# Optimization experiments

Hardware: AMD Instinct MI355X
Metric: run time of the kernel (lower is better)

## Reference

```python
import jax, jax.numpy as jnp
import numpy as np

N_NODES = 50000
N_EDGES = 600000
D = 128
THETA = (0.5, -1.0, 0.5)  # len(theta) must be 3 to match learnable_diag[3, in_feats]


def setup_inputs() -> dict:
    key = jax.random.key(0)
    k1, k2, k3, k4, k5 = jax.random.split(key, 5)
    feat = jax.random.normal(k1, (N_NODES, D), dtype=jnp.float32)
    edge_index = jax.random.randint(k2, (2, N_EDGES), 0, N_NODES)  # [src; dst]
    # learnable_diag = torch.rand(3, in_feats)
    diag = jax.random.uniform(k3, (3, D), dtype=jnp.float32)
    # nn.Linear(out_feats, out_feats) with xavier_uniform weight, zero bias
    limit = float(np.sqrt(6.0 / (D + D)))
    W = jax.random.uniform(k4, (D, D), dtype=jnp.float32, minval=-limit, maxval=limit)
    b = jnp.zeros((D,), dtype=jnp.float32)
    return {"feat": feat, "edge_index": edge_index, "diag": diag, "W": W, "b": b}


def reference(feat, edge_index, diag, W, b):
    src, dst = edge_index[0], edge_index[1]
    n = feat.shape[0]
    # in_degrees: count of incoming edges per node
    deg = jax.ops.segment_sum(jnp.ones_like(dst, dtype=feat.dtype), dst, num_segments=n)
    d_invsqrt = jnp.clip(deg, 1.0, None) ** -0.5  # [N]
    d_invsqrt = d_invsqrt[:, None]  # [N,1]

    h = (THETA[0] * feat) * diag[0]
    h = h @ W.T + b  # nn.Linear

    for k in range(1, len(THETA)):
        # unnLaplacian: feat - (A @ (feat * Dinv)) * Dinv * diag[k]
        msg = feat * d_invsqrt  # [N,D]
        agg = jax.ops.segment_sum(msg[src], dst, num_segments=n)  # SpMM: copy_u + sum
        feat = feat - agg * d_invsqrt * diag[k]
        h = h + THETA[k] * feat
    return h
```

## Files before the change

### kernel.cpp

```cpp
#include <hip/hip_runtime.h>

#define NN 50000
#define NE 600000
#define D  128
#define NBLK 196

typedef __attribute__((ext_vector_type(8))) short bf16x8;
typedef __attribute__((ext_vector_type(4))) float floatx4;

__device__ __forceinline__ unsigned short bf16_rne(float f) {
    union { float f; unsigned u; } v; v.f = f;
    unsigned r = v.u + 0x7FFFu + ((v.u >> 16) & 1u);
    return (unsigned short)(r >> 16);
}

__global__ __launch_bounds__(256) void hist_kernel(const int* __restrict__ dst,
                                                   int* __restrict__ deg_i) {
    int e = blockIdx.x * 256 + threadIdx.x;
    if (e < NE) atomicAdd(&deg_i[dst[e]], 1);
}

__global__ __launch_bounds__(256) void scan1_kernel(const int* __restrict__ deg_i,
                                                    int* __restrict__ row_ptr,
                                                    int* __restrict__ partials,
                                                    float* __restrict__ dinvf) {
    __shared__ int sh[256];
    int i = blockIdx.x * 256 + threadIdx.x;
    int dg = (i < NN) ? deg_i[i] : 0;
    if (i < NN) {
        float d = (float)dg;
        dinvf[i] = rsqrtf(d > 1.0f ? d : 1.0f);
    }
    sh[threadIdx.x] = dg;
    __syncthreads();
    #pragma unroll
    for (int off = 1; off < 256; off <<= 1) {
        int t = (threadIdx.x >= off) ? sh[threadIdx.x - off] : 0;
        __syncthreads();
        sh[threadIdx.x] += t;
        __syncthreads();
    }
    if (i < NN) row_ptr[i + 1] = sh[threadIdx.x];
    if (threadIdx.x == 255) partials[blockIdx.x] = sh[255];
}

__global__ __launch_bounds__(256) void scan2_kernel(int* __restrict__ partials) {
    __shared__ int sh[256];
    sh[threadIdx.x] = (threadIdx.x < NBLK) ? partials[threadIdx.x] : 0;
    __syncthreads();
    #pragma unroll
    for (int off = 1; off < 256; off <<= 1) {
        int t = (threadIdx.x >= off) ? sh[threadIdx.x - off] : 0;
        __syncthreads();
        sh[threadIdx.x] += t;
        __syncthreads();
    }
    if (threadIdx.x < NBLK) partials[threadIdx.x] = sh[threadIdx.x];
}

__global__ __launch_bounds__(256) void scan3_kernel(int* __restrict__ row_ptr,
                                                    const int* __restrict__ partials,
                                                    int* __restrict__ fillc) {
    int i = blockIdx.x * 256 + threadIdx.x;
    if (i < NN) {
        int add = (blockIdx.x > 0) ? partials[blockIdx.x - 1] : 0;
        row_ptr[i + 1] += add;
        fillc[i] = 0;
    }
    if (i == 0) row_ptr[0] = 0;
}

__global__ __launch_bounds__(256) void fill_kernel(const int* __restrict__ src,
                                                   const int* __restrict__ dst,
                                                   const int* __restrict__ row_ptr,
                                                   const float* __restrict__ dinvf,
                                                   int* __restrict__ fillc,
                                                   int2* __restrict__ csr) {
    int e = blockIdx.x * 256 + threadIdx.x;
    if (e < NE) {
        int t = dst[e];
        int s = src[e];
        int pos = row_ptr[t] + atomicAdd(&fillc[t], 1);
        csr[pos] = make_int2(s, __float_as_int(dinvf[s]));
    }
}

__global__ __launch_bounds__(256) void cvt_kernel(const float* __restrict__ feat,
                                                  unsigned int* __restrict__ featb) {
    int idx = blockIdx.x * 256 + threadIdx.x;
    const float4 f = ((const float4*)feat)[idx];
    unsigned int lo = (unsigned)bf16_rne(f.x) | ((unsigned)bf16_rne(f.y) << 16);
    unsigned int hi = (unsigned)bf16_rne(f.z) | ((unsigned)bf16_rne(f.w) << 16);
    ((uint2*)featb)[idx] = make_uint2(lo, hi);
}

__device__ __forceinline__ float2 gather_acc(const unsigned short* __restrict__ featb,
                                             const int2* __restrict__ csr,
                                             int e0, int e1, int lane) {
    float2 acc = make_float2(0.0f, 0.0f);
    for (int bse = e0; bse < e1; bse += 64) {
        int idx = bse + lane;
        int s = 0;
        float w = 0.0f;
        if (idx < e1) {
            int2 p = csr[idx];
            s = p.x;
            w = __int_as_float(p.y);
        }
        int cnt4 = (min(64, e1 - bse) + 3) & ~3;
        for (int k = 0; k < cnt4; k += 4) {
            #pragma unroll
            for (int u = 0; u < 4; ++u) {
                int   ss = __shfl(s, k + u);
                float ww = __shfl(w, k + u);
                unsigned pv = *(const unsigned*)(featb + (size_t)ss * D + 2 * lane);
                acc.x += __uint_as_float(pv << 16) * ww;
                acc.y += __uint_as_float(pv & 0xFFFF0000u) * ww;
            }
        }
    }
    return acc;
}

__global__ __launch_bounds__(256) void gather1_kernel(const unsigned short* __restrict__ featb,
                                                      const int2* __restrict__ csr,
                                                      const int* __restrict__ row_ptr,
                                                      const float* __restrict__ dinvf,
                                                      const float* __restrict__ diag,
                                                      const float* __restrict__ feat0,
                                                      unsigned int* __restrict__ feat1b) {
    const int node = blockIdx.x * 4 + (threadIdx.x >> 6);
    const int lane = threadIdx.x & 63;
    float2 acc = gather_acc(featb, csr, row_ptr[node], row_ptr[node + 1], lane);

    const size_t o2 = (size_t)node * (D / 2) + lane;
    const float di = dinvf[node];
    const float2 bs = *(const float2*)&feat0[2 * o2];
    const float2 dg = *(const float2*)&diag[D + 2 * lane];
    float rx = bs.x - acc.x * di * dg.x;
    float ry = bs.y - acc.y * di * dg.y;
    feat1b[o2] = (unsigned)bf16_rne(rx) | ((unsigned)bf16_rne(ry) << 16);
}

__global__ __launch_bounds__(256) void gather2_kernel(const unsigned short* __restrict__ feat1b,
                                                      const int2* __restrict__ csr,
                                                      const int* __restrict__ row_ptr,
                                                      const float* __restrict__ dinvf,
                                                      const float* __restrict__ diag,
                                                      float* __restrict__ outp) {
    const int node = blockIdx.x * 4 + (threadIdx.x >> 6);
    const int lane = threadIdx.x & 63;
    float2 acc = gather_acc(feat1b, csr, row_ptr[node], row_ptr[node + 1], lane);

    const size_t o2 = (size_t)node * (D / 2) + lane;
    const float di = dinvf[node];
    const unsigned bp = ((const unsigned*)feat1b)[o2];
    const float2 dg = *(const float2*)&diag[2 * D + 2 * lane];
    float bx = __uint_as_float(bp << 16);
    float by = __uint_as_float(bp & 0xFFFF0000u);
    float2 r;
    r.x = -0.5f * (bx + acc.x * di * dg.x);
    r.y = -0.5f * (by + acc.y * di * dg.y);
    *(float2*)&outp[2 * o2] = r;
}

__global__ __launch_bounds__(256) void wprep_kernel(const float* __restrict__ W,
                                                    const float* __restrict__ diag,
                                                    unsigned short* __restrict__ Wb) {
    int idx = blockIdx.x * 256 + threadIdx.x;
    int j = idx & 127;
    Wb[idx] = bf16_rne(0.5f * diag[j] * W[idx]);
}

__global__ __launch_bounds__(256) void gemm_mfma_kernel(const float* __restrict__ feat,
                                                        const unsigned short* __restrict__ Wb,
                                                        const float* __restrict__ b,
                                                        float* __restrict__ out) {
    const int wv   = threadIdx.x >> 6;
    const int lane = threadIdx.x & 63;
    const int r16  = lane & 15;
    const int quad = lane >> 4;
    const int m0   = blockIdx.x * 64 + wv * 16;

    const int mrow = m0 + r16;
    const int mc   = (mrow < NN) ? mrow : (NN - 1);
    const float* arow = feat + (size_t)mc * D + quad * 8;

    bf16x8 afrag[4];
    #pragma unroll
    for (int kc = 0; kc < 4; ++kc) {
        const float4 f0 = *(const float4*)(arow + kc * 32);
        const float4 f1 = *(const float4*)(arow + kc * 32 + 4);
        bf16x8 a;
        a[0] = (short)bf16_rne(f0.x); a[1] = (short)bf16_rne(f0.y);
        a[2] = (short)bf16_rne(f0.z); a[3] = (short)bf16_rne(f0.w);
        a[4] = (short)bf16_rne(f1.x); a[5] = (short)bf16_rne(f1.y);
        a[6] = (short)bf16_rne(f1.z); a[7] = (short)bf16_rne(f1.w);
        afrag[kc] = a;
    }

    floatx4 acc[8];
    #pragma unroll
    for (int nt = 0; nt < 8; ++nt) acc[nt] = (floatx4)(0.0f);

    #pragma unroll
    for (int nt = 0; nt < 8; ++nt) {
        const unsigned short* brow = Wb + (size_t)(nt * 16 + r16) * D + quad * 8;
        #pragma unroll
        for (int kc = 0; kc < 4; ++kc) {
            const bf16x8 bfrag = *(const bf16x8*)(brow + kc * 32);
            acc[nt] = __builtin_amdgcn_mfma_f32_16x16x32_bf16(afrag[kc], bfrag, acc[nt], 0, 0, 0);
        }
    }

    #pragma unroll
    for (int nt = 0; nt < 8; ++nt) {
        const int d = nt * 16 + r16;
        const float bd = b[d];
        #pragma unroll
        for (int r = 0; r < 4; ++r) {
            const int i = m0 + quad * 4 + r;
            if (i < NN) {
                const size_t o = (size_t)i * D + d;
                out[o] = acc[nt][r] + bd + out[o];
            }
        }
    }
}

extern "C" void kernel_launch(void* const* d_in, const int* in_sizes, int n_in,
                              void* d_out, int out_size, void* d_ws, size_t ws_size,
                              hipStream_t stream) {
    const float* feat = (const float*)d_in[0];
    const int*   eidx = (const int*)d_in[1];
    const float* diag = (const float*)d_in[2];
    const float* W    = (const float*)d_in[3];
    const float* b    = (const float*)d_in[4];
    float* out = (float*)d_out;

    const int* src = eidx;
    const int* dst = eidx + NE;

    unsigned short* featb  = (unsigned short*)d_ws;
    unsigned short* feat1b = featb + (size_t)NN * D;
    int2*  csr      = (int2*)(feat1b + (size_t)NN * D);
    float* dinvf    = (float*)(csr + NE);
    int*   deg_i    = (int*)(dinvf + NN);
    int*   row_ptr  = deg_i + NN;
    int*   fillc    = row_ptr + NN + 2;
    int*   partials = fillc + NN;
    unsigned short* Wb = (unsigned short*)(partials + 256);

    hipMemsetAsync(deg_i, 0, (size_t)NN * sizeof(int), stream);

    hist_kernel<<<(NE + 255) / 256, 256, 0, stream>>>(dst, deg_i);
    scan1_kernel<<<NBLK, 256, 0, stream>>>(deg_i, row_ptr, partials, dinvf);
    scan2_kernel<<<1, 256, 0, stream>>>(partials);
    scan3_kernel<<<NBLK, 256, 0, stream>>>(row_ptr, partials, fillc);
    fill_kernel<<<(NE + 255) / 256, 256, 0, stream>>>(src, dst, row_ptr, dinvf, fillc, csr);

    cvt_kernel<<<NN * D / 4 / 256, 256, 0, stream>>>(feat, (unsigned int*)featb);
    wprep_kernel<<<64, 256, 0, stream>>>(W, diag, Wb);

    gather1_kernel<<<NN / 4, 256, 0, stream>>>(featb, csr, row_ptr, dinvf, diag,
                                               feat, (unsigned int*)feat1b);
    gather2_kernel<<<NN / 4, 256, 0, stream>>>(feat1b, csr, row_ptr, dinvf, diag, out);

    gemm_mfma_kernel<<<(NN + 63) / 64, 256, 0, stream>>>(feat, Wb, b, out);
}
```

Measured before the change: 240.4 us.

## Prescale source rows by inverse sqrt degree and fuse bf16 conversion into GEMM

Stores bf16 feature rows already multiplied by each source node's inverse sqrt degree. The CSR entries can then shrink to a single int index with no per-edge weight. The bf16 conversion kernel is removed and folded into the GEMM, which now runs first, writes the bias output, and is accumulated into by gather2. Gather loops are unrolled by 8, padded indices point to a zeroed sentinel row, and rdeg is kept so feat1 can be unscaled; this adds extra rounding from storing the scaled values in bf16.

```diff
diff --git a/kernel.cpp b/kernel.cpp
--- a/kernel.cpp
+++ b/kernel.cpp
@@ -13,6 +13,9 @@
     unsigned r = v.u + 0x7FFFu + ((v.u >> 16) & 1u);
     return (unsigned short)(r >> 16);
 }
+__device__ __forceinline__ unsigned pack2(float a, float b) {
+    return (unsigned)bf16_rne(a) | ((unsigned)bf16_rne(b) << 16);
+}
 
 __global__ __launch_bounds__(256) void hist_kernel(const int* __restrict__ dst,
                                                    int* __restrict__ deg_i) {
@@ -23,13 +26,16 @@
 __global__ __launch_bounds__(256) void scan1_kernel(const int* __restrict__ deg_i,
                                                     int* __restrict__ row_ptr,
                                                     int* __restrict__ partials,
-                                                    float* __restrict__ dinvf) {
+                                                    float* __restrict__ dinvf,
+                                                    float* __restrict__ rdegf) {
     __shared__ int sh[256];
     int i = blockIdx.x * 256 + threadIdx.x;
     int dg = (i < NN) ? deg_i[i] : 0;
     if (i < NN) {
         float d = (float)dg;
-        dinvf[i] = rsqrtf(d > 1.0f ? d : 1.0f);
+        float dc = d > 1.0f ? d : 1.0f;
+        dinvf[i] = rsqrtf(dc);
+        rdegf[i] = sqrtf(dc);
     }
     sh[threadIdx.x] = dg;
     __syncthreads();
@@ -73,95 +79,14 @@
 __global__ __launch_bounds__(256) void fill_kernel(const int* __restrict__ src,
                                                    const int* __restrict__ dst,
                                                    const int* __restrict__ row_ptr,
-                                                   const float* __restrict__ dinvf,
                                                    int* __restrict__ fillc,
-                                                   int2* __restrict__ csr) {
+                                                   int* __restrict__ csr) {
     int e = blockIdx.x * 256 + threadIdx.x;
     if (e < NE) {
         int t = dst[e];
-        int s = src[e];
         int pos = row_ptr[t] + atomicAdd(&fillc[t], 1);
-        csr[pos] = make_int2(s, __float_as_int(dinvf[s]));
-    }
-}
-
-__global__ __launch_bounds__(256) void cvt_kernel(const float* __restrict__ feat,
-                                                  unsigned int* __restrict__ featb) {
-    int idx = blockIdx.x * 256 + threadIdx.x;
-    const float4 f = ((const float4*)feat)[idx];
-    unsigned int lo = (unsigned)bf16_rne(f.x) | ((unsigned)bf16_rne(f.y) << 16);
-    unsigned int hi = (unsigned)bf16_rne(f.z) | ((unsigned)bf16_rne(f.w) << 16);
-    ((uint2*)featb)[idx] = make_uint2(lo, hi);
-}
-
-__device__ __forceinline__ float2 gather_acc(const unsigned short* __restrict__ featb,
-                                             const int2* __restrict__ csr,
-                                             int e0, int e1, int lane) {
-    float2 acc = make_float2(0.0f, 0.0f);
-    for (int bse = e0; bse < e1; bse += 64) {
-        int idx = bse + lane;
-        int s = 0;
-        float w = 0.0f;
-        if (idx < e1) {
-            int2 p = csr[idx];
-            s = p.x;
-            w = __int_as_float(p.y);
-        }
-        int cnt4 = (min(64, e1 - bse) + 3) & ~3;
-        for (int k = 0; k < cnt4; k += 4) {
-            #pragma unroll
-            for (int u = 0; u < 4; ++u) {
-                int   ss = __shfl(s, k + u);
-                float ww = __shfl(w, k + u);
-                unsigned pv = *(const unsigned*)(featb + (size_t)ss * D + 2 * lane);
-                acc.x += __uint_as_float(pv << 16) * ww;
-                acc.y += __uint_as_float(pv & 0xFFFF0000u) * ww;
-            }
-        }
-    }
-    return acc;
-}
-
-__global__ __launch_bounds__(256) void gather1_kernel(const unsigned short* __restrict__ featb,
-                                                      const int2* __restrict__ csr,
-                                                      const int* __restrict__ row_ptr,
-                                                      const float* __restrict__ dinvf,
-                                                      const float* __restrict__ diag,
-                                                      const float* __restrict__ feat0,
-                                                      unsigned int* __restrict__ feat1b) {
-    const int node = blockIdx.x * 4 + (threadIdx.x >> 6);
-    const int lane = threadIdx.x & 63;
-    float2 acc = gather_acc(featb, csr, row_ptr[node], row_ptr[node + 1], lane);
-
-    const size_t o2 = (size_t)node * (D / 2) + lane;
-    const float di = dinvf[node];
-    const float2 bs = *(const float2*)&feat0[2 * o2];
-    const float2 dg = *(const float2*)&diag[D + 2 * lane];
-    float rx = bs.x - acc.x * di * dg.x;
-    float ry = bs.y - acc.y * di * dg.y;
-    feat1b[o2] = (unsigned)bf16_rne(rx) | ((unsigned)bf16_rne(ry) << 16);
-}
-
-__global__ __launch_bounds__(256) void gather2_kernel(const unsigned short* __restrict__ feat1b,
-                                                      const int2* __restrict__ csr,
-                                                      const int* __restrict__ row_ptr,
-                                                      const float* __restrict__ dinvf,
-                                                      const float* __restrict__ diag,
-                                                      float* __restrict__ outp) {
-    const int node = blockIdx.x * 4 + (threadIdx.x >> 6);
-    const int lane = threadIdx.x & 63;
-    float2 acc = gather_acc(feat1b, csr, row_ptr[node], row_ptr[node + 1], lane);
-
-    const size_t o2 = (size_t)node * (D / 2) + lane;
-    const float di = dinvf[node];
-    const unsigned bp = ((const unsigned*)feat1b)[o2];
-    const float2 dg = *(const float2*)&diag[2 * D + 2 * lane];
-    float bx = __uint_as_float(bp << 16);
-    float by = __uint_as_float(bp & 0xFFFF0000u);
-    float2 r;
-    r.x = -0.5f * (bx + acc.x * di * dg.x);
-    r.y = -0.5f * (by + acc.y * di * dg.y);
-    *(float2*)&outp[2 * o2] = r;
+        csr[pos] = src[e];
+    }
 }
 
 __global__ __launch_bounds__(256) void wprep_kernel(const float* __restrict__ W,
@@ -175,6 +100,8 @@
 __global__ __launch_bounds__(256) void gemm_mfma_kernel(const float* __restrict__ feat,
                                                         const unsigned short* __restrict__ Wb,
                                                         const float* __restrict__ b,
+                                                        const float* __restrict__ dinvf,
+                                                        unsigned short* __restrict__ featb_s,
                                                         float* __restrict__ out) {
     const int wv   = threadIdx.x >> 6;
     const int lane = threadIdx.x & 63;
@@ -185,6 +112,7 @@
     const int mrow = m0 + r16;
     const int mc   = (mrow < NN) ? mrow : (NN - 1);
     const float* arow = feat + (size_t)mc * D + quad * 8;
+    const float di = dinvf[mc];
 
     bf16x8 afrag[4];
     #pragma unroll
@@ -197,6 +125,14 @@
         a[4] = (short)bf16_rne(f1.x); a[5] = (short)bf16_rne(f1.y);
         a[6] = (short)bf16_rne(f1.z); a[7] = (short)bf16_rne(f1.w);
         afrag[kc] = a;
+        if (mrow < NN) {
+            uint4 st;
+            st.x = pack2(f0.x * di, f0.y * di);
+            st.y = pack2(f0.z * di, f0.w * di);
+            st.z = pack2(f1.x * di, f1.y * di);
+            st.w = pack2(f1.z * di, f1.w * di);
+            *(uint4*)(featb_s + (size_t)mc * D + quad * 8 + kc * 32) = st;
+        }
     }
 
     floatx4 acc[8];
@@ -220,12 +156,74 @@
         #pragma unroll
         for (int r = 0; r < 4; ++r) {
             const int i = m0 + quad * 4 + r;
-            if (i < NN) {
-                const size_t o = (size_t)i * D + d;
-                out[o] = acc[nt][r] + bd + out[o];
+            if (i < NN) out[(size_t)i * D + d] = acc[nt][r] + bd;
+        }
+    }
+}
+
+__device__ __forceinline__ float2 gather_acc(const unsigned short* __restrict__ rows,
+                                             const int* __restrict__ csr,
+                                             int e0, int e1, int lane) {
+    float2 acc = make_float2(0.0f, 0.0f);
+    for (int bse = e0; bse < e1; bse += 64) {
+        int idx = bse + lane;
+        int s = (idx < e1) ? csr[idx] : NN;
+        int cnt8 = (min(64, e1 - bse) + 7) & ~7;
+        for (int k = 0; k < cnt8; k += 8) {
+            #pragma unroll
+            for (int u = 0; u < 8; ++u) {
+                int ss = __shfl(s, k + u);
+                unsigned pv = *(const unsigned*)(rows + (size_t)ss * D + 2 * lane);
+                acc.x += __uint_as_float(pv << 16);
+                acc.y += __uint_as_float(pv & 0xFFFF0000u);
             }
         }
     }
+    return acc;
+}
+
+__global__ __launch_bounds__(256) void gather1_kernel(const unsigned short* __restrict__ featb_s,
+                                                      const int* __restrict__ csr,
+                                                      const int* __restrict__ row_ptr,
+                                                      const float* __restrict__ dinvf,
+                                                      const float* __restrict__ diag,
+                                                      const float* __restrict__ feat0,
+                                                      unsigned int* __restrict__ feat1s) {
+    const int node = blockIdx.x * 4 + (threadIdx.x >> 6);
+    const int lane = threadIdx.x & 63;
+    float2 acc = gather_acc(featb_s, csr, row_ptr[node], row_ptr[node + 1], lane);
+
+    const size_t o2 = (size_t)node * (D / 2) + lane;
+    const float di = dinvf[node];
+    const float2 bs = *(const float2*)&feat0[2 * o2];
+    const float2 dg = *(const float2*)&diag[D + 2 * lane];
+    float rx = bs.x - acc.x * di * dg.x;
+    float ry = bs.y - acc.y * di * dg.y;
+    feat1s[o2] = pack2(rx * di, ry * di);
+}
+
+__global__ __launch_bounds__(256) void gather2_kernel(const unsigned short* __restrict__ feat1s,
+                                                      const int* __restrict__ csr,
+                                                      const int* __restrict__ row_ptr,
+                                                      const float* __restrict__ dinvf,
+                                                      const float* __restrict__ rdegf,
+                                                      const float* __restrict__ diag,
+                                                      float* __restrict__ outp) {
+    const int node = blockIdx.x * 4 + (threadIdx.x >> 6);
+    const int lane = threadIdx.x & 63;
+    float2 acc = gather_acc(feat1s, csr, row_ptr[node], row_ptr[node + 1], lane);
+
+    const size_t o2 = (size_t)node * (D / 2) + lane;
+    const float di = dinvf[node];
+    const float rd = rdegf[node];
+    const unsigned bp = ((const unsigned*)feat1s)[o2];
+    const float2 dg = *(const float2*)&diag[2 * D + 2 * lane];
+    float bx = __uint_as_float(bp << 16) * rd;
+    float by = __uint_as_float(bp & 0xFFFF0000u) * rd;
+    float2 cur = *(const float2*)&outp[2 * o2];
+    cur.x -= 0.5f * (bx + acc.x * di * dg.x);
+    cur.y -= 0.5f * (by + acc.y * di * dg.y);
+    *(float2*)&outp[2 * o2] = cur;
 }
 
 extern "C" void kernel_launch(void* const* d_in, const int* in_sizes, int n_in,
@@ -241,30 +239,32 @@
     const int* src = eidx;
     const int* dst = eidx + NE;
 
-    unsigned short* featb  = (unsigned short*)d_ws;
-    unsigned short* feat1b = featb + (size_t)NN * D;
-    int2*  csr      = (int2*)(feat1b + (size_t)NN * D);
+    unsigned short* featb_s = (unsigned short*)d_ws;
+    unsigned short* feat1s  = featb_s + (size_t)(NN + 1) * D;
+    int*   csr      = (int*)(feat1s + (size_t)(NN + 1) * D);
     float* dinvf    = (float*)(csr + NE);
-    int*   deg_i    = (int*)(dinvf + NN);
+    float* rdegf    = dinvf + NN;
+    int*   deg_i    = (int*)(rdegf + NN);
     int*   row_ptr  = deg_i + NN;
     int*   fillc    = row_ptr + NN + 2;
     int*   partials = fillc + NN;
     unsigned short* Wb = (unsigned short*)(partials + 256);
 
     hipMemsetAsync(deg_i, 0, (size_t)NN * sizeof(int), stream);
+    hipMemsetAsync(featb_s + (size_t)NN * D, 0, D * sizeof(unsigned short), stream);
+    hipMemsetAsync(feat1s  + (size_t)NN * D, 0, D * sizeof(unsigned short), stream);
 
     hist_kernel<<<(NE + 255) / 256, 256, 0, stream>>>(dst, deg_i);
-    scan1_kernel<<<NBLK, 256, 0, stream>>>(deg_i, row_ptr, partials, dinvf);
+    scan1_kernel<<<NBLK, 256, 0, stream>>>(deg_i, row_ptr, partials, dinvf, rdegf);
     scan2_kernel<<<1, 256, 0, stream>>>(partials);
     scan3_kernel<<<NBLK, 256, 0, stream>>>(row_ptr, partials, fillc);
-    fill_kernel<<<(NE + 255) / 256, 256, 0, stream>>>(src, dst, row_ptr, dinvf, fillc, csr);
-
-    cvt_kernel<<<NN * D / 4 / 256, 256, 0, stream>>>(feat, (unsigned int*)featb);
+    fill_kernel<<<(NE + 255) / 256, 256, 0, stream>>>(src, dst, row_ptr, fillc, csr);
+
     wprep_kernel<<<64, 256, 0, stream>>>(W, diag, Wb);
 
-    gather1_kernel<<<NN / 4, 256, 0, stream>>>(featb, csr, row_ptr, dinvf, diag,
-                                               feat, (unsigned int*)feat1b);
-    gather2_kernel<<<NN / 4, 256, 0, stream>>>(feat1b, csr, row_ptr, dinvf, diag, out);
-
-    gemm_mfma_kernel<<<(NN + 63) / 64, 256, 0, stream>>>(feat, Wb, b, out);
-}
+    gemm_mfma_kernel<<<(NN + 63) / 64, 256, 0, stream>>>(feat, Wb, b, dinvf, featb_s, out);
+
+    gather1_kernel<<<NN / 4, 256, 0, stream>>>(featb_s, csr, row_ptr, dinvf, diag,
+                                               feat, (unsigned int*)feat1s);
+    gather2_kernel<<<NN / 4, 256, 0, stream>>>(feat1s, csr, row_ptr, dinvf, rdegf, diag, out);
+}
```

Measured after the change: 235.3 us. 1.02x faster.
